# Kernel tuning notes

Hardware: AMD Instinct MI355X
Metric: run time of the kernel (lower is better)

Reference implementation:

```python
import jax, jax.numpy as jnp
import numpy as np

EPS = 1e-5


def setup_inputs() -> dict:
    key = jax.random.key(0)
    ks = jax.random.split(key, 8)
    Ns, E, F, H, O = 8192, 200000, 20, 1024, 2
    N = Ns + E
    return {
        "state": jax.random.normal(ks[0], (Ns, F), dtype=jnp.float32),
        "edge_attr": jax.random.normal(ks[1], (E, F), dtype=jnp.float32),
        "edge_index": jax.random.randint(ks[2], (2, E), 0, N, dtype=jnp.int64),
        "W_gcn": jax.random.normal(ks[3], (F, H), dtype=jnp.float32) * 0.05,
        "b_gcn": jax.random.normal(ks[4], (H,), dtype=jnp.float32) * 0.05,
        "gamma": jnp.ones((H,), dtype=jnp.float32),
        "beta": jnp.zeros((H,), dtype=jnp.float32),
        "W_lin": jax.random.normal(ks[5], (H, O), dtype=jnp.float32) * 0.05,
        "b_lin": jnp.zeros((O,), dtype=jnp.float32),
    }


def gcn_conv(x, edge_index, W, b):
    # PyG GCNConv: add self-loops, symmetric deg^{-1/2} normalization,
    # linear transform, sum-aggregate src -> dst, add bias.
    N = x.shape[0]
    loop = jnp.arange(N, dtype=edge_index.dtype)
    src = jnp.concatenate([edge_index[0], loop])
    dst = jnp.concatenate([edge_index[1], loop])
    deg = jnp.zeros((N,), dtype=x.dtype).at[dst].add(1.0)  # >=1 from self-loops
    dinv = jax.lax.rsqrt(deg)
    norm = dinv[src] * dinv[dst]                 # [E+N]
    xw = x @ W                                   # [N, H]
    msg = xw[src] * norm[:, None]                # [E+N, H] gather + scale
    out = jax.ops.segment_sum(msg, dst, num_segments=N)  # scatter-add
    return out + b


def reference(state, edge_attr, edge_index, W_gcn, b_gcn, gamma, beta, W_lin, b_lin):
    # node features = cat(state, edge_attr) along node dim
    node_features = jnp.concatenate([state, edge_attr], axis=0)  # [N, 20]
    h = gcn_conv(node_features, edge_index, W_gcn, b_gcn)        # [N, 1024]
    # BatchNorm1d (train-mode: batch statistics, biased variance)
    mean = jnp.mean(h, axis=0)
    var = jnp.mean(jnp.square(h - mean), axis=0)
    h = (h - mean) * jax.lax.rsqrt(var + EPS) * gamma + beta
    # Linear -> ReLU -> Softmax(dim=1)
    logits = jax.nn.relu(h @ W_lin + b_lin)                      # [N, 2]
    return jax.nn.softmax(logits, axis=1)
```

## Files before the change

### kernel.cpp

```cpp
#include <hip/hip_runtime.h>


#define F 20
#define NSTAT 230
#define SROWS 256
#define BSZ 256

__global__ void k_init(float* __restrict__ deg, float4* __restrict__ y4,
                       float* __restrict__ stats, int N) {
  int i = blockIdx.x * blockDim.x + threadIdx.x;
  if (i < N * 5) y4[i] = make_float4(0.f, 0.f, 0.f, 0.f);
  if (i < N) deg[i] = 1.0f;
  if (i < 256) stats[i] = 0.f;
}

__global__ void k_deg_acc(const int* __restrict__ dst, float* __restrict__ deg, int E) {
  int e = blockIdx.x * blockDim.x + threadIdx.x;
  if (e < E) atomicAdd(&deg[dst[e]], 1.0f);
}

__global__ void k_scatter(const int* __restrict__ src, const int* __restrict__ dst,
                          const float* __restrict__ deg,
                          const float* __restrict__ state,
                          const float* __restrict__ edge_attr,
                          float* __restrict__ y, int E, int Ns) {
  int tid = blockIdx.x * blockDim.x + threadIdx.x;
  if (tid >= E * F) return;
  int e = tid / F;
  int f = tid - e * F;
  int s = src[e];
  int d = dst[e];
  float norm = rsqrtf(deg[s]) * rsqrtf(deg[d]);
  int xi = s * F + f;
  int sb = Ns * F;
  float x = (xi < sb) ? state[xi] : edge_attr[xi - sb];
  atomicAdd(&y[(size_t)d * F + f], norm * x);
}

__global__ __launch_bounds__(BSZ) void k_stats(
    const float* __restrict__ state, const float* __restrict__ edge_attr,
    const float* __restrict__ deg, float* __restrict__ y,
    float* __restrict__ stats, int N, int Ns) {
  __shared__ float lds[SROWS * F];
  int t = threadIdx.x;

  long rowbase = (long)blockIdx.x * SROWS;
  for (int i4 = t; i4 < SROWS * 5; i4 += BSZ) {
    int rl = i4 / 5;
    int q = i4 - rl * 5;
    long row = rowbase + rl;
    float4 v = make_float4(0.f, 0.f, 0.f, 0.f);
    if (row < N) {
      long gi = row * F + q * 4;
      float4 ye = *reinterpret_cast<const float4*>(y + gi);
      const float* xrow = (row < (long)Ns) ? (state + row * F)
                                           : (edge_attr + (row - Ns) * F);
      float4 xv = *reinterpret_cast<const float4*>(xrow + q * 4);
      float di = 1.0f / deg[row];
      v.x = ye.x + xv.x * di;
      v.y = ye.y + xv.y * di;
      v.z = ye.z + xv.z * di;
      v.w = ye.w + xv.w * di;
      *reinterpret_cast<float4*>(y + gi) = v;
    }
    *reinterpret_cast<float4*>(lds + i4 * 4) = v;
  }
  __syncthreads();

  if (t < F) {
    float a0 = 0.f, a1 = 0.f, a2 = 0.f, a3 = 0.f;
    for (int r = 0; r < SROWS; r += 4) {
      a0 += lds[(r + 0) * F + t];
      a1 += lds[(r + 1) * F + t];
      a2 += lds[(r + 2) * F + t];
      a3 += lds[(r + 3) * F + t];
    }
    atomicAdd(&stats[t], (a0 + a1) + (a2 + a3));
  } else if (t < NSTAT) {
    int k = t - F, i = 0;
    while (k >= F - i) { k -= F - i; i++; }
    int ci = i, cj = i + k;
    float a0 = 0.f, a1 = 0.f, a2 = 0.f, a3 = 0.f;
    for (int r = 0; r < SROWS; r += 4) {
      a0 += lds[(r + 0) * F + ci] * lds[(r + 0) * F + cj];
      a1 += lds[(r + 1) * F + ci] * lds[(r + 1) * F + cj];
      a2 += lds[(r + 2) * F + ci] * lds[(r + 2) * F + cj];
      a3 += lds[(r + 3) * F + ci] * lds[(r + 3) * F + cj];
    }
    atomicAdd(&stats[t], (a0 + a1) + (a2 + a3));
  }
}

__global__ __launch_bounds__(256, 1) void k_finalize(
    const float* __restrict__ stats,
    const float* __restrict__ W_gcn,
    const float* __restrict__ gamma,
    const float* __restrict__ beta,
    const float* __restrict__ W_lin,
    const float* __restrict__ b_lin,
    float* __restrict__ params,
    int N, int H) {
  __shared__ float Cu_s[210];
  __shared__ float ybar_s[F];
  __shared__ float part[4][44];
  int t = threadIdx.x;
  int lane = t & 63;
  int wv = t >> 6;
  float invN = 1.0f / (float)N;
  if (t < F) ybar_s[t] = stats[t] * invN;
  __syncthreads();
  if (t < 210) {
    int k = t, i = 0;
    while (k >= F - i) { k -= F - i; i++; }
    int j = i + k;
    float cv = stats[F + t] * invN - ybar_s[i] * ybar_s[j];
    Cu_s[t] = (i == j) ? cv : 2.0f * cv;
  }
  __syncthreads();

  float m0[F], m1[F];
  #pragma unroll
  for (int f = 0; f < F; ++f) { m0[f] = 0.f; m1[f] = 0.f; }
  float d0 = 0.f, d1 = 0.f;

  for (int hb = 0; hb < H; hb += 4 * 256) {
    float w[4][F];
    float var[4];
    int hh[4];
    bool act[4];
    #pragma unroll
    for (int c = 0; c < 4; ++c) {
      int h = hb + c * 256 + t;
      act[c] = (h < H);
      hh[c] = act[c] ? h : 0;
      var[c] = 0.f;
      #pragma unroll
      for (int f = 0; f < F; ++f) {
        float x = W_gcn[f * H + hh[c]];
        w[c][f] = act[c] ? x : 0.f;
      }
    }
    int p = 0;
    #pragma unroll
    for (int i = 0; i < F; ++i) {
      #pragma unroll
      for (int j = i; j < F; ++j) {
        float cu = Cu_s[p];
        ++p;
        #pragma unroll
        for (int c = 0; c < 4; ++c) var[c] += cu * (w[c][i] * w[c][j]);
      }
    }
    #pragma unroll
    for (int c = 0; c < 4; ++c) {
      float sg = act[c] ? (gamma[hh[c]] * rsqrtf(var[c] + 1e-5f)) : 0.f;
      float wl0 = W_lin[hh[c] * 2 + 0], wl1 = W_lin[hh[c] * 2 + 1];
      float s0 = sg * wl0, s1 = sg * wl1;
      #pragma unroll
      for (int f = 0; f < F; ++f) { m0[f] += w[c][f] * s0; m1[f] += w[c][f] * s1; }
      float bt = act[c] ? beta[hh[c]] : 0.f;
      d0 += bt * wl0;
      d1 += bt * wl1;
    }
  }

  #pragma unroll
  for (int f = 0; f < F; ++f) {
    float v0 = m0[f], v1 = m1[f];
    #pragma unroll
    for (int off = 32; off; off >>= 1) {
      v0 += __shfl_xor(v0, off);
      v1 += __shfl_xor(v1, off);
    }
    if (lane == 0) { part[wv][2 * f] = v0; part[wv][2 * f + 1] = v1; }
  }
  #pragma unroll
  for (int off = 32; off; off >>= 1) {
    d0 += __shfl_xor(d0, off);
    d1 += __shfl_xor(d1, off);
  }
  if (lane == 0) { part[wv][40] = d0; part[wv][41] = d1; }
  __syncthreads();

  if (t < 42) {
    float acc = 0.f;
    for (int w2 = 0; w2 < 4; ++w2) acc += part[w2][t];
    if (t >= 40) acc += b_lin[t - 40];
    params[t] = acc;
  } else if (t < 62) {
    params[t] = ybar_s[t - 42];
  }
}

__global__ void k_out(const float* __restrict__ y,
                      const float* __restrict__ params,
                      float* __restrict__ out, int N) {
  __shared__ float P[64];
  if (threadIdx.x < 62) P[threadIdx.x] = params[threadIdx.x];
  __syncthreads();
  int n = blockIdx.x * blockDim.x + threadIdx.x;
  if (n >= N) return;
  const float4* yr4 = reinterpret_cast<const float4*>(y + (size_t)n * F);
  float l0 = P[40], l1 = P[41];
  #pragma unroll
  for (int k = 0; k < 5; ++k) {
    float4 q = yr4[k];
    float vv[4] = {q.x, q.y, q.z, q.w};
    #pragma unroll
    for (int u = 0; u < 4; ++u) {
      int f = 4 * k + u;
      float dv = vv[u] - P[42 + f];
      l0 += dv * P[2 * f + 0];
      l1 += dv * P[2 * f + 1];
    }
  }
  l0 = fmaxf(l0, 0.f);
  l1 = fmaxf(l1, 0.f);
  float m = fmaxf(l0, l1);
  float e0 = __expf(l0 - m), e1 = __expf(l1 - m);
  float inv = 1.0f / (e0 + e1);
  float2 o2;
  o2.x = e0 * inv;
  o2.y = e1 * inv;
  reinterpret_cast<float2*>(out)[n] = o2;
}

extern "C" void kernel_launch(void* const* d_in, const int* in_sizes, int n_in,
                              void* d_out, int out_size, void* d_ws, size_t ws_size,
                              hipStream_t stream) {
  const float* state     = (const float*)d_in[0];
  const float* edge_attr = (const float*)d_in[1];
  const int*   eidx      = (const int*)d_in[2];
  const float* W_gcn     = (const float*)d_in[3];
  const float* gamma     = (const float*)d_in[5];
  const float* beta      = (const float*)d_in[6];
  const float* W_lin     = (const float*)d_in[7];
  const float* b_lin     = (const float*)d_in[8];
  float* out = (float*)d_out;

  int Ns = in_sizes[0] / F;
  int E  = in_sizes[2] / 2;
  int N  = Ns + in_sizes[1] / F;
  int H  = in_sizes[4];

  const int* src = eidx;
  const int* dst = eidx + E;

  float* ws     = (float*)d_ws;
  float* deg    = ws;
  float* y      = ws + N;
  float* stats  = y + (size_t)N * F;
  float* params = stats + 256;

  int nblk = (N + SROWS - 1) / SROWS;

  k_init<<<(N * 5 + BSZ - 1) / BSZ, BSZ, 0, stream>>>(deg, (float4*)y, stats, N);
  k_deg_acc<<<(E + BSZ - 1) / BSZ, BSZ, 0, stream>>>(dst, deg, E);
  k_scatter<<<(E * F + BSZ - 1) / BSZ, BSZ, 0, stream>>>(
      src, dst, deg, state, edge_attr, y, E, Ns);
  k_stats<<<nblk, BSZ, 0, stream>>>(state, edge_attr, deg, y, stats, N, Ns);
  k_finalize<<<1, 256, 0, stream>>>(stats, W_gcn, gamma, beta, W_lin, b_lin,
                                    params, N, H);
  k_out<<<(N + BSZ - 1) / BSZ, BSZ, 0, stream>>>(y, params, out, N);
}
```

Baseline: 104.8 us.

## Bucket edges by destination tile and aggregate in shared memory

Replaces the global-atomic scatter of edge messages with a counting sort of edges into 256-row destination buckets (count, scan, fill). Each tile block then accumulates its incoming messages with shared-memory atomics and fuses the self-loop, the normalization and the statistics. This removes the zeroing of y and the contention-heavy global float atomics on y. It adds three small kernels, a single-block scan and an edge index buffer. Bucket sizes are uneven, so block load can be imbalanced, and one 1024-thread scan block limits NB to 1024 buckets.

```diff
diff --git a/kernel.cpp b/kernel.cpp
--- a/kernel.cpp
+++ b/kernel.cpp
@@ -6,43 +6,84 @@
 #define SROWS 256
 #define BSZ 256
 
-__global__ void k_init(float* __restrict__ deg, float4* __restrict__ y4,
-                       float* __restrict__ stats, int N) {
+__global__ void k_init(float* __restrict__ deg, float* __restrict__ stats,
+                       int* __restrict__ counts, int N, int NB) {
   int i = blockIdx.x * blockDim.x + threadIdx.x;
-  if (i < N * 5) y4[i] = make_float4(0.f, 0.f, 0.f, 0.f);
-  if (i < N) deg[i] = 1.0f;
+  if (i < N) deg[i] = 0.f;
   if (i < 256) stats[i] = 0.f;
-}
-
-__global__ void k_deg_acc(const int* __restrict__ dst, float* __restrict__ deg, int E) {
+  if (i < NB) counts[i] = 0;
+}
+
+__global__ void k_deg_count(const int* __restrict__ dst, float* __restrict__ deg,
+                            int* __restrict__ counts, int E) {
   int e = blockIdx.x * blockDim.x + threadIdx.x;
-  if (e < E) atomicAdd(&deg[dst[e]], 1.0f);
-}
-
-__global__ void k_scatter(const int* __restrict__ src, const int* __restrict__ dst,
-                          const float* __restrict__ deg,
-                          const float* __restrict__ state,
-                          const float* __restrict__ edge_attr,
-                          float* __restrict__ y, int E, int Ns) {
-  int tid = blockIdx.x * blockDim.x + threadIdx.x;
-  if (tid >= E * F) return;
-  int e = tid / F;
-  int f = tid - e * F;
-  int s = src[e];
+  if (e >= E) return;
   int d = dst[e];
-  float norm = rsqrtf(deg[s]) * rsqrtf(deg[d]);
-  int xi = s * F + f;
+  atomicAdd(&deg[d], 1.0f);
+  atomicAdd(&counts[d >> 8], 1);
+}
+
+__global__ __launch_bounds__(1024) void k_scan(const int* __restrict__ counts,
+                                               int* __restrict__ bstart,
+                                               int* __restrict__ cursor,
+                                               int NB, int E) {
+  __shared__ int s[1024];
+  int t = threadIdx.x;
+  int c = (t < NB) ? counts[t] : 0;
+  s[t] = c;
+  __syncthreads();
+  for (int off = 1; off < 1024; off <<= 1) {
+    int v = (t >= off) ? s[t - off] : 0;
+    __syncthreads();
+    s[t] += v;
+    __syncthreads();
+  }
+  if (t < NB) {
+    int excl = s[t] - c;
+    bstart[t] = excl;
+    cursor[t] = excl;
+  }
+  if (t == 0) bstart[NB] = E;
+}
+
+__global__ void k_fill(const int* __restrict__ dst, int* __restrict__ cursor,
+                       int* __restrict__ ebuf, int E) {
+  int e = blockIdx.x * blockDim.x + threadIdx.x;
+  if (e >= E) return;
+  int c = dst[e] >> 8;
+  int pos = atomicAdd(&cursor[c], 1);
+  ebuf[pos] = e;
+}
+
+__global__ __launch_bounds__(BSZ) void k_tile(
+    const int* __restrict__ src, const int* __restrict__ dst,
+    const int* __restrict__ bstart, const int* __restrict__ ebuf,
+    const float* __restrict__ deg,
+    const float* __restrict__ state, const float* __restrict__ edge_attr,
+    float* __restrict__ y, float* __restrict__ stats, int N, int Ns) {
+  __shared__ float tile[SROWS * F];
+  int t = threadIdx.x;
+
+  for (int i4 = t; i4 < SROWS * 5; i4 += BSZ)
+    *reinterpret_cast<float4*>(tile + i4 * 4) = make_float4(0.f, 0.f, 0.f, 0.f);
+  __syncthreads();
+
+  int start = bstart[blockIdx.x];
+  int cnt = bstart[blockIdx.x + 1] - start;
   int sb = Ns * F;
-  float x = (xi < sb) ? state[xi] : edge_attr[xi - sb];
-  atomicAdd(&y[(size_t)d * F + f], norm * x);
-}
-
-__global__ __launch_bounds__(BSZ) void k_stats(
-    const float* __restrict__ state, const float* __restrict__ edge_attr,
-    const float* __restrict__ deg, float* __restrict__ y,
-    float* __restrict__ stats, int N, int Ns) {
-  __shared__ float lds[SROWS * F];
-  int t = threadIdx.x;
+  int nit = cnt * F;
+  for (int it = t; it < nit; it += BSZ) {
+    int le = it / F;
+    int f = it - le * F;
+    int e = ebuf[start + le];
+    int s = src[e];
+    int d = dst[e];
+    float ns = rsqrtf(deg[s] + 1.0f);
+    int xi = s * F + f;
+    float x = (xi < sb) ? state[xi] : edge_attr[xi - sb];
+    atomicAdd(&tile[(d & (SROWS - 1)) * F + f], ns * x);
+  }
+  __syncthreads();
 
   long rowbase = (long)blockIdx.x * SROWS;
   for (int i4 = t; i4 < SROWS * 5; i4 += BSZ) {
@@ -51,29 +92,28 @@
     long row = rowbase + rl;
     float4 v = make_float4(0.f, 0.f, 0.f, 0.f);
     if (row < N) {
-      long gi = row * F + q * 4;
-      float4 ye = *reinterpret_cast<const float4*>(y + gi);
+      float4 zv = *reinterpret_cast<const float4*>(tile + i4 * 4);
       const float* xrow = (row < (long)Ns) ? (state + row * F)
                                            : (edge_attr + (row - Ns) * F);
       float4 xv = *reinterpret_cast<const float4*>(xrow + q * 4);
-      float di = 1.0f / deg[row];
-      v.x = ye.x + xv.x * di;
-      v.y = ye.y + xv.y * di;
-      v.z = ye.z + xv.z * di;
-      v.w = ye.w + xv.w * di;
-      *reinterpret_cast<float4*>(y + gi) = v;
-    }
-    *reinterpret_cast<float4*>(lds + i4 * 4) = v;
+      float di = rsqrtf(deg[row] + 1.0f);
+      v.x = di * (zv.x + di * xv.x);
+      v.y = di * (zv.y + di * xv.y);
+      v.z = di * (zv.z + di * xv.z);
+      v.w = di * (zv.w + di * xv.w);
+      *reinterpret_cast<float4*>(y + row * F + q * 4) = v;
+    }
+    *reinterpret_cast<float4*>(tile + i4 * 4) = v;
   }
   __syncthreads();
 
   if (t < F) {
     float a0 = 0.f, a1 = 0.f, a2 = 0.f, a3 = 0.f;
     for (int r = 0; r < SROWS; r += 4) {
-      a0 += lds[(r + 0) * F + t];
-      a1 += lds[(r + 1) * F + t];
-      a2 += lds[(r + 2) * F + t];
-      a3 += lds[(r + 3) * F + t];
+      a0 += tile[(r + 0) * F + t];
+      a1 += tile[(r + 1) * F + t];
+      a2 += tile[(r + 2) * F + t];
+      a3 += tile[(r + 3) * F + t];
     }
     atomicAdd(&stats[t], (a0 + a1) + (a2 + a3));
   } else if (t < NSTAT) {
@@ -82,10 +122,10 @@
     int ci = i, cj = i + k;
     float a0 = 0.f, a1 = 0.f, a2 = 0.f, a3 = 0.f;
     for (int r = 0; r < SROWS; r += 4) {
-      a0 += lds[(r + 0) * F + ci] * lds[(r + 0) * F + cj];
-      a1 += lds[(r + 1) * F + ci] * lds[(r + 1) * F + cj];
-      a2 += lds[(r + 2) * F + ci] * lds[(r + 2) * F + cj];
-      a3 += lds[(r + 3) * F + ci] * lds[(r + 3) * F + cj];
+      a0 += tile[(r + 0) * F + ci] * tile[(r + 0) * F + cj];
+      a1 += tile[(r + 1) * F + ci] * tile[(r + 1) * F + cj];
+      a2 += tile[(r + 2) * F + ci] * tile[(r + 2) * F + cj];
+      a3 += tile[(r + 3) * F + ci] * tile[(r + 3) * F + cj];
     }
     atomicAdd(&stats[t], (a0 + a1) + (a2 + a3));
   }
@@ -246,19 +286,24 @@
   const int* src = eidx;
   const int* dst = eidx + E;
 
+  int NB = (N + SROWS - 1) / SROWS;
+
   float* ws     = (float*)d_ws;
   float* deg    = ws;
   float* y      = ws + N;
   float* stats  = y + (size_t)N * F;
   float* params = stats + 256;
-
-  int nblk = (N + SROWS - 1) / SROWS;
-
-  k_init<<<(N * 5 + BSZ - 1) / BSZ, BSZ, 0, stream>>>(deg, (float4*)y, stats, N);
-  k_deg_acc<<<(E + BSZ - 1) / BSZ, BSZ, 0, stream>>>(dst, deg, E);
-  k_scatter<<<(E * F + BSZ - 1) / BSZ, BSZ, 0, stream>>>(
-      src, dst, deg, state, edge_attr, y, E, Ns);
-  k_stats<<<nblk, BSZ, 0, stream>>>(state, edge_attr, deg, y, stats, N, Ns);
+  int*   counts = (int*)(params + 64);
+  int*   bstart = counts + NB;
+  int*   cursor = bstart + NB + 1;
+  int*   ebuf   = cursor + NB;
+
+  k_init<<<(N + BSZ - 1) / BSZ, BSZ, 0, stream>>>(deg, stats, counts, N, NB);
+  k_deg_count<<<(E + BSZ - 1) / BSZ, BSZ, 0, stream>>>(dst, deg, counts, E);
+  k_scan<<<1, 1024, 0, stream>>>(counts, bstart, cursor, NB, E);
+  k_fill<<<(E + BSZ - 1) / BSZ, BSZ, 0, stream>>>(dst, cursor, ebuf, E);
+  k_tile<<<NB, BSZ, 0, stream>>>(src, dst, bstart, ebuf, deg, state, edge_attr,
+                                 y, stats, N, Ns);
   k_finalize<<<1, 256, 0, stream>>>(stats, W_gcn, gamma, beta, W_lin, b_lin,
                                     params, N, H);
   k_out<<<(N + BSZ - 1) / BSZ, BSZ, 0, stream>>>(y, params, out, N);
```

Result: slower. 202.3 us (+93.0%).
